# Kernel optimization log

Measured on AMD Instinct MI355X. Metric: run time of the kernel, lower is better.

## Reference

```python
import jax, jax.numpy as jnp
from jax import lax
import numpy as np

EPS = 1e-5

def setup_inputs() -> dict:
    key = jax.random.key(0)
    k1, k2, k3, k4 = jax.random.split(key, 4)
    B, in_c, out_c, k, z_dim, H, W = 16, 128, 256, 3, 256, 64, 64
    fan_in = in_c * k * k
    x = jax.random.normal(k1, (B, in_c, H, W), dtype=jnp.float32)
    z = jax.random.normal(k2, (B, z_dim), dtype=jnp.float32)
    base_weight = jax.random.normal(k3, (out_c, in_c, k, k), dtype=jnp.float32) * np.sqrt(2.0 / fan_in)
    head_w = jax.random.normal(k4, (out_c * in_c * k * k, z_dim), dtype=jnp.float32) * np.sqrt(1.0 / z_dim)
    return {"x": x, "z": z, "base_weight": base_weight, "head_w": head_w}

def reference(x, z, base_weight, head_w):
    # x: [B, in_c, H, W]; z: [B, z_dim]; base_weight: [out_c, in_c, k, k]; head_w: [out_c*in_c*k*k, z_dim]
    B = x.shape[0]
    out_c, in_c, k, _ = base_weight.shape
    fan_in = in_c * k * k
    hyper_weight = 1.0

    # delta_w = Linear(z) -> [B, out_c, in_c, k, k]
    delta_w = jnp.einsum('bz,oz->bo', z, head_w).reshape(B, out_c, in_c, k, k)
    # standardize over (in_c, k, k) per (sample, out-channel)
    mu = jnp.mean(delta_w, axis=(2, 3, 4), keepdims=True)
    var = jnp.var(delta_w, axis=(2, 3, 4), keepdims=True)
    delta_w = (delta_w - mu) * lax.rsqrt(var + EPS)
    delta_w = delta_w * jnp.sqrt(2.0 / fan_in)

    w = (base_weight[None] + hyper_weight * delta_w) / jnp.sqrt(2.0)  # [B, out_c, in_c, k, k]

    pad = k // 2
    def conv_one(xb, wb):
        # xb: [in_c, H, W], wb: [out_c, in_c, k, k]
        return lax.conv_general_dilated(
            xb[None], wb, window_strides=(1, 1), padding=[(pad, pad), (pad, pad)],
            dimension_numbers=('NCHW', 'OIHW', 'NCHW'))[0]

    out = jax.vmap(conv_one)(x, w)  # [B, out_c, H_out, W_out]
    return out
```

## Files before the change

kernel.cpp:

```cpp
#include <hip/hip_runtime.h>

#define B_  16
#define IC  128
#define OC  256
#define ZD  256
#define HH  64
#define WW  64
#define FAN 1152
#define NO  294912
#define HP  66

typedef float    fvec4 __attribute__((ext_vector_type(4)));
typedef _Float16 f16x8 __attribute__((ext_vector_type(8)));
typedef _Float16 f16x4 __attribute__((ext_vector_type(4)));

__global__ __launch_bounds__(256) void delta_gemm_kernel(
    const float* __restrict__ z, const float* __restrict__ head_w,
    float* __restrict__ delta) {
  __shared__ _Float16 As[256 * 72];
  __shared__ _Float16 zsh[16 * 264];
  int t = threadIdx.x;
  int row0 = blockIdx.x * 256;
  int lane = t & 63, wave = t >> 6;
  int quad = lane >> 4, l16 = lane & 15;

  for (int u = t; u < 1024; u += 256) {
    int b = u >> 6, kq = u & 63;
    fvec4 v = *(const fvec4*)&z[b * 256 + kq * 4];
    f16x4 h = {(_Float16)v.x, (_Float16)v.y, (_Float16)v.z, (_Float16)v.w};
    *(f16x4*)&zsh[b * 264 + kq * 4] = h;
  }

  fvec4 acc[4];
#pragma unroll
  for (int i = 0; i < 4; ++i) acc[i] = (fvec4){0.f, 0.f, 0.f, 0.f};

  int srow_lo = t >> 4;
  int sseg = t & 15;

  for (int zc2 = 0; zc2 < 4; ++zc2) {
    __syncthreads();
#pragma unroll
    for (int i = 0; i < 16; ++i) {
      int row = i * 16 + srow_lo;
      fvec4 v = *(const fvec4*)&head_w[(size_t)(row0 + row) * 256 + zc2 * 64 + sseg * 4];
      f16x4 h = {(_Float16)v.x, (_Float16)v.y, (_Float16)v.z, (_Float16)v.w};
      *(f16x4*)&As[row * 72 + sseg * 4] = h;
    }
    __syncthreads();
#pragma unroll
    for (int kc = 0; kc < 2; ++kc) {
      f16x8 bfz = *(const f16x8*)&zsh[l16 * 264 + zc2 * 64 + kc * 32 + quad * 8];
#pragma unroll
      for (int mt = 0; mt < 4; ++mt) {
        f16x8 af = *(const f16x8*)&As[(wave * 64 + mt * 16 + l16) * 72 + kc * 32 + quad * 8];
        acc[mt] = __builtin_amdgcn_mfma_f32_16x16x32_f16(af, bfz, acc[mt], 0, 0, 0);
      }
    }
  }
#pragma unroll
  for (int mt = 0; mt < 4; ++mt) {
    int gr = row0 + wave * 64 + mt * 16 + quad * 4;
#pragma unroll
    for (int r = 0; r < 4; ++r)
      delta[(size_t)l16 * NO + gr + r] = acc[mt][r];
  }
}

__global__ __launch_bounds__(256) void standardize_kernel(
    const float* __restrict__ delta, const float* __restrict__ base_w,
    _Float16* __restrict__ w_h) {
  int b  = blockIdx.x >> 8;
  int oc = blockIdx.x & 255;
  int tid = threadIdx.x;
  const float* d = delta + (size_t)b * NO + oc * FAN;

  float s = 0.f, s2 = 0.f;
  for (int j = tid; j < FAN; j += 256) { float v = d[j]; s += v; s2 += v * v; }
#pragma unroll
  for (int off = 32; off > 0; off >>= 1) {
    s  += __shfl_down(s, off);
    s2 += __shfl_down(s2, off);
  }
  __shared__ float rs[4], rq[4];
  if ((tid & 63) == 0) { rs[tid >> 6] = s; rq[tid >> 6] = s2; }
  __syncthreads();
  float S  = rs[0] + rs[1] + rs[2] + rs[3];
  float S2 = rq[0] + rq[1] + rq[2] + rq[3];
  const float inv_fan = 1.0f / (float)FAN;
  float mu  = S * inv_fan;
  float var = S2 * inv_fan - mu * mu;
  const float inv_sqrt2 = 0.70710678118654752f;
  float sc = rsqrtf(var + 1e-5f) * sqrtf(2.0f / (float)FAN) * inv_sqrt2;

  const float* bw = base_w + oc * FAN;
  _Float16* wp = w_h + ((size_t)b * OC + oc) * FAN;
  for (int i = tid; i < FAN; i += 256) {
    int ic = i & 127, kk = i >> 7;
    int j = ic * 9 + kk;
    float val = bw[j] * inv_sqrt2 + (d[j] - mu) * sc;
    wp[i] = (_Float16)val;
  }
}

__global__ __launch_bounds__(256) void xpose_kernel(
    const float* __restrict__ x, _Float16* __restrict__ x_h) {
  int yp = blockIdx.x;
  int b  = blockIdx.y;
  int t  = threadIdx.x;
  _Float16* orow = x_h + ((size_t)(b * HP + yp)) * HP * IC;

  if (yp == 0 || yp == HP - 1) {
    fvec4 zz = (fvec4){0.f, 0.f, 0.f, 0.f};
    for (int u = t; u < HP * IC / 8; u += 256)
      ((fvec4*)orow)[u] = zz;
    return;
  }
  int y = yp - 1;
  __shared__ float tile[128 * 65];
#pragma unroll
  for (int i = 0; i < 8; ++i) {
    int F = i * 256 + t;
    int ic = F >> 4, xq = F & 15;
    fvec4 v = *(const fvec4*)&x[(((size_t)b * IC + ic) * HH + y) * WW + xq * 4];
    float* tp = &tile[ic * 65 + xq * 4];
    tp[0] = v.x; tp[1] = v.y; tp[2] = v.z; tp[3] = v.w;
  }
  __syncthreads();
#pragma unroll
  for (int j = 0; j < 4; ++j) {
    int u = j * 256 + t;
    int px = u >> 4, icg = u & 15;
    _Float16 h[8];
#pragma unroll
    for (int c = 0; c < 8; ++c) h[c] = (_Float16)tile[(icg * 8 + c) * 65 + px];
    *(f16x8*)&orow[(px + 1) * IC + icg * 8] = *(f16x8*)h;
  }
  if (t < 32) {
    int side = t >> 4, icg = t & 15;
    fvec4 zz = (fvec4){0.f, 0.f, 0.f, 0.f};
    *(fvec4*)&orow[(side ? (HP - 1) * IC : 0) + icg * 8] = zz;
  }
}

__global__ __launch_bounds__(256) void conv_mfma_kernel(
    const _Float16* __restrict__ x_h, const _Float16* __restrict__ w_h,
    float* __restrict__ out) {
  int t = threadIdx.x;
  int b = blockIdx.z;
  int oc0 = blockIdx.y * 128;
  int y0 = blockIdx.x * 2;
  int lane = t & 63, wave = t >> 6;
  int wm = wave >> 1, wn = wave & 1;
  int quad = lane >> 4, l16 = lane & 15;

  fvec4 acc[4][4];
#pragma unroll
  for (int i = 0; i < 4; ++i)
#pragma unroll
    for (int j = 0; j < 4; ++j) acc[i][j] = (fvec4){0.f, 0.f, 0.f, 0.f};

  const _Float16* ap = w_h + ((size_t)(b * OC + oc0 + wm * 64 + l16)) * FAN + quad * 8;
  const _Float16* bp = x_h + (((size_t)(b * HP + y0 + wn)) * HP + l16) * IC + quad * 8;

#pragma unroll
  for (int ky = 0; ky < 3; ++ky) {
#pragma unroll
    for (int kx = 0; kx < 3; ++kx) {
      int kk = ky * 3 + kx;
      const _Float16* apk = ap + kk * 128;
      const _Float16* bpk = bp + (ky * HP + kx) * IC;
#pragma unroll
      for (int icc = 0; icc < 2; ++icc) {
#pragma unroll
        for (int ks = 0; ks < 2; ++ks) {
          f16x8 af[4], bf[4];
#pragma unroll
          for (int i = 0; i < 4; ++i)
            af[i] = *(const f16x8*)(apk + i * (16 * FAN) + icc * 64 + ks * 32);
#pragma unroll
          for (int j = 0; j < 4; ++j)
            bf[j] = *(const f16x8*)(bpk + j * (16 * IC) + icc * 64 + ks * 32);
#pragma unroll
          for (int i = 0; i < 4; ++i)
#pragma unroll
            for (int j = 0; j < 4; ++j)
              acc[i][j] = __builtin_amdgcn_mfma_f32_16x16x32_f16(af[i], bf[j], acc[i][j], 0, 0, 0);
        }
      }
    }
  }

#pragma unroll
  for (int i = 0; i < 4; ++i)
#pragma unroll
    for (int j = 0; j < 4; ++j) {
      int m  = oc0 + wm * 64 + i * 16 + quad * 4;
      int nn = wn * 64 + j * 16 + l16;
      int oy = y0 + (nn >> 6), ox = nn & 63;
      float* op = out + (((size_t)(b * OC + m) * HH + oy) * WW + ox);
#pragma unroll
      for (int r = 0; r < 4; ++r)
        op[(size_t)r * HH * WW] = acc[i][j][r];
    }
}

extern "C" void kernel_launch(void* const* d_in, const int* in_sizes, int n_in,
                              void* d_out, int out_size, void* d_ws, size_t ws_size,
                              hipStream_t stream) {
  const float* x      = (const float*)d_in[0];
  const float* z      = (const float*)d_in[1];
  const float* base_w = (const float*)d_in[2];
  const float* head_w = (const float*)d_in[3];
  float* out = (float*)d_out;

  _Float16* w_h   = (_Float16*)d_ws;
  float*    delta = (float*)((char*)d_ws + (size_t)B_ * OC * FAN * sizeof(_Float16));
  _Float16* x_h   = (_Float16*)delta;

  delta_gemm_kernel<<<NO / 256, 256, 0, stream>>>(z, head_w, delta);
  standardize_kernel<<<B_ * OC, 256, 0, stream>>>(delta, base_w, w_h);
  xpose_kernel<<<dim3(HP, B_), 256, 0, stream>>>(x, x_h);
  conv_mfma_kernel<<<dim3(32, 2, B_), 256, 0, stream>>>(x_h, w_h, out);
}
```

Measured before the change: 589.5 us.

## Stage conv operand tiles in LDS via direct global-to-LDS loads with XOR swizzle

```diff
diff --git a/kernel.cpp b/kernel.cpp
--- a/kernel.cpp
+++ b/kernel.cpp
@@ -13,6 +13,13 @@
 typedef float    fvec4 __attribute__((ext_vector_type(4)));
 typedef _Float16 f16x8 __attribute__((ext_vector_type(8)));
 typedef _Float16 f16x4 __attribute__((ext_vector_type(4)));
+
+__device__ __forceinline__ void gl_lds16(const _Float16* g, _Float16* ldst) {
+  __builtin_amdgcn_global_load_lds(
+      (const __attribute__((address_space(1))) unsigned int*)(const void*)g,
+      (__attribute__((address_space(3))) unsigned int*)(void*)ldst,
+      16, 0, 0);
+}
 
 __global__ __launch_bounds__(256) void delta_gemm_kernel(
     const float* __restrict__ z, const float* __restrict__ head_w,
@@ -146,6 +153,8 @@
 __global__ __launch_bounds__(256) void conv_mfma_kernel(
     const _Float16* __restrict__ x_h, const _Float16* __restrict__ w_h,
     float* __restrict__ out) {
+  __shared__ __align__(16) _Float16 As[128 * 64];
+  __shared__ __align__(16) _Float16 Bs[128 * 64];
   int t = threadIdx.x;
   int b = blockIdx.z;
   int oc0 = blockIdx.y * 128;
@@ -160,27 +169,55 @@
 #pragma unroll
     for (int j = 0; j < 4; ++j) acc[i][j] = (fvec4){0.f, 0.f, 0.f, 0.f};
 
-  const _Float16* ap = w_h + ((size_t)(b * OC + oc0 + wm * 64 + l16)) * FAN + quad * 8;
-  const _Float16* bp = x_h + (((size_t)(b * HP + y0 + wn)) * HP + l16) * IC + quad * 8;
+  int lrow = lane >> 3;
+  int lseg = lane & 7;
+  int sw   = lseg ^ lrow;
+
+  const _Float16* apg[4];
+#pragma unroll
+  for (int n = 0; n < 4; ++n)
+    apg[n] = w_h + ((size_t)(b * OC + oc0 + wave * 32 + n * 8 + lrow)) * FAN + sw * 8;
+
+  const _Float16* bpg0 =
+      x_h + (((size_t)(b * HP + y0 + (wave >> 1))) * HP + (wave & 1) * 32 + lrow) * IC + sw * 8;
+  const _Float16* bpg1 = bpg0 + 16 * IC;
+
+  _Float16* adst = As + wave * 32 * 64;
+  _Float16* bdst = Bs + wave * 32 * 64;
+
+  int s7 = l16 & 7;
+  int arow = (wm * 64 + l16) * 64;
+  int brow = (wn * 64 + l16) * 64;
+  int aoff[2] = { arow + ((0 + quad) ^ s7) * 8, arow + ((4 + quad) ^ s7) * 8 };
+  int boff[2] = { brow + ((0 + quad) ^ s7) * 8, brow + ((4 + quad) ^ s7) * 8 };
 
 #pragma unroll
   for (int ky = 0; ky < 3; ++ky) {
 #pragma unroll
     for (int kx = 0; kx < 3; ++kx) {
-      int kk = ky * 3 + kx;
-      const _Float16* apk = ap + kk * 128;
-      const _Float16* bpk = bp + (ky * HP + kx) * IC;
+      const int kk = ky * 3 + kx;
+      const _Float16* b0k = bpg0 + (ky * HP + kx) * IC;
+      const _Float16* b1k = bpg1 + (ky * HP + kx) * IC;
 #pragma unroll
       for (int icc = 0; icc < 2; ++icc) {
+        __syncthreads();
+#pragma unroll
+        for (int n = 0; n < 4; ++n)
+          gl_lds16(apg[n] + kk * 128 + icc * 64, adst + n * 512);
+        gl_lds16(b0k + icc * 64,        bdst);
+        gl_lds16(b0k + 1024 + icc * 64, bdst + 512);
+        gl_lds16(b1k + icc * 64,        bdst + 1024);
+        gl_lds16(b1k + 1024 + icc * 64, bdst + 1536);
+        __syncthreads();
 #pragma unroll
         for (int ks = 0; ks < 2; ++ks) {
           f16x8 af[4], bf[4];
 #pragma unroll
           for (int i = 0; i < 4; ++i)
-            af[i] = *(const f16x8*)(apk + i * (16 * FAN) + icc * 64 + ks * 32);
+            af[i] = *(const f16x8*)&As[aoff[ks] + i * 1024];
 #pragma unroll
           for (int j = 0; j < 4; ++j)
-            bf[j] = *(const f16x8*)(bpk + j * (16 * IC) + icc * 64 + ks * 32);
+            bf[j] = *(const f16x8*)&Bs[boff[ks] + j * 1024];
 #pragma unroll
           for (int i = 0; i < 4; ++i)
 #pragma unroll
@@ -216,7 +253,8 @@
 
   _Float16* w_h   = (_Float16*)d_ws;
   float*    delta = (float*)((char*)d_ws + (size_t)B_ * OC * FAN * sizeof(_Float16));
-  _Float16* x_h   = (_Float16*)delta;
+  _Float16* x_h   = (_Float16*)((char*)d_ws + (size_t)B_ * OC * FAN * sizeof(_Float16)
+                                            + (size_t)B_ * NO * sizeof(float));
 
   delta_gemm_kernel<<<NO / 256, 256, 0, stream>>>(z, head_w, delta);
   standardize_kernel<<<B_ * OC, 256, 0, stream>>>(delta, base_w, w_h);
```

Measured after the change: 510.2 us. 1.16x faster.
